# Performance work log

Measured on AMD Instinct MI355X. Metric: run time of the kernel, lower is better.

The kernel has to match this reference:

```python
import jax, jax.numpy as jnp
import numpy as np


def dwconv1d(u, w, b):
    # u: (B, C, L), w: (C, 1, 3) depthwise, padding=1 -> same length
    out = jax.lax.conv_general_dilated(
        u, w, window_strides=(1,), padding=[(1, 1)],
        dimension_numbers=('NCH', 'OIH', 'NCH'),
        feature_group_count=u.shape[1])
    return out + b[None, :, None]


def selective_scan(u, delta, A, Bm, Cm, D, delta_bias):
    # u, delta: (B, KD, L); A: (KD, N); Bm, Cm: (B, K, N, L); D, delta_bias: (KD,)
    Bsz, KD, L = u.shape
    K, N = Bm.shape[1], Bm.shape[2]
    Dg = KD // K
    delta = jax.nn.softplus(delta + delta_bias[None, :, None])
    Bexp = jnp.repeat(Bm, Dg, axis=1)  # (B, KD, N, L)
    Cexp = jnp.repeat(Cm, Dg, axis=1)
    dA = jnp.exp(delta[:, :, None, :] * A[None, :, :, None])        # (B, KD, N, L)
    dBu = delta[:, :, None, :] * Bexp * u[:, :, None, :]            # (B, KD, N, L)

    def step(h, inp):
        a, bu, c = inp
        h = a * h + bu
        return h, jnp.sum(h * c, axis=-1)

    a_t = jnp.moveaxis(dA, -1, 0)
    bu_t = jnp.moveaxis(dBu, -1, 0)
    c_t = jnp.moveaxis(Cexp, -1, 0)
    _, ys = jax.lax.scan(step, jnp.zeros((Bsz, KD, N), u.dtype), (a_t, bu_t, c_t))
    return jnp.moveaxis(ys, 0, -1) + D[None, :, None] * u           # (B, KD, L)


def setup_inputs():
    key = jax.random.key(0)
    ks = jax.random.split(key, 8)
    d_inner, d_state, dt_rank, K = 192, 16, 6, 1
    bincounts = np.array([4096, 3000, 3500, 2500])
    total = int(bincounts.sum())
    max_bin = int(bincounts.max())
    starts = np.concatenate([[0], np.cumsum(bincounts)[:-1]])
    # compute_padding: wrap-around padded gather indices per cloud
    padded_idx = np.concatenate([np.arange(max_bin) % bc + st for bc, st in zip(bincounts, starts)])
    # crop-back indices into the (B*max_bin) padded layout
    valid_idx = np.concatenate([i * max_bin + np.arange(bc) for i, bc in enumerate(bincounts)])
    order = np.stack([np.random.RandomState(0).permutation(total)])
    inverse = np.argsort(order, axis=1)
    x = jax.random.normal(ks[0], (d_inner, total), jnp.float32)
    x_proj_weight = jax.random.normal(ks[1], (K, dt_rank + 2 * d_state, d_inner), jnp.float32) * 0.05
    dt_projs_weight = jax.random.normal(ks[2], (K, d_inner, dt_rank), jnp.float32) * 0.1
    dt_projs_bias = jax.random.normal(ks[3], (K, d_inner), jnp.float32) * 0.1
    A_logs = jnp.log(jnp.tile(jnp.arange(1, d_state + 1, dtype=jnp.float32), (K * d_inner, 1)))
    Ds = jnp.ones((K * d_inner,), jnp.float32)
    conv_w = jax.random.normal(ks[4], (K * d_inner, 1, 3), jnp.float32) * 0.2
    conv_b = jnp.zeros((K * d_inner,), jnp.float32)
    ln_gamma = jnp.ones((d_inner,), jnp.float32)
    ln_beta = jnp.zeros((d_inner,), jnp.float32)
    return {
        'x': x, 'x_proj_weight': x_proj_weight, 'dt_projs_weight': dt_projs_weight,
        'dt_projs_bias': dt_projs_bias, 'A_logs': A_logs, 'Ds': Ds,
        'conv_w': conv_w, 'conv_b': conv_b, 'ln_gamma': ln_gamma, 'ln_beta': ln_beta,
        'order': jnp.asarray(order, jnp.int32), 'inverse': jnp.asarray(inverse, jnp.int32),
        'padded_idx': jnp.asarray(padded_idx, jnp.int32),
        'valid_idx': jnp.asarray(valid_idx, jnp.int32), 'max_bin': max_bin,
    }


def reference(x, x_proj_weight, dt_projs_weight, dt_projs_bias, A_logs, Ds,
              conv_w, conv_b, ln_gamma, ln_beta,
              order, inverse, padded_idx, valid_idx, max_bin):
    K, Dch, R = dt_projs_weight.shape
    N = A_logs.shape[1]
    BM = padded_idx.shape[0]
    Bsz = BM // max_bin
    # multi-directional gather with offset padding: x[:, order[k]][:, padded_idx]
    idx = jnp.take(order, padded_idx, axis=1)                       # (K, B*max_bin)
    xs = jnp.take(x, idx, axis=1)                                   # (Dch, K, B*max_bin)
    xs = xs.transpose(1, 0, 2).reshape(K, Dch, Bsz, max_bin).transpose(2, 0, 1, 3)  # (B,K,D,L)
    x_dbl = jnp.einsum('bkdl,kcd->bkcl', xs, x_proj_weight)         # (B,K,R+2N,L)
    dts, Bs, Cs = jnp.split(x_dbl, [R, R + N], axis=2)
    dts = jnp.einsum('bkrl,kdr->bkdl', dts, dt_projs_weight)
    u = xs.reshape(Bsz, K * Dch, max_bin)
    delta = dts.reshape(Bsz, K * Dch, max_bin)
    A = -jnp.exp(A_logs)
    u = dwconv1d(u, conv_w, conv_b)  # conv1d applied after x_dbl/dts, before scan
    ys = selective_scan(u, delta, A, Bs, Cs, Ds, dt_projs_bias.reshape(-1))  # (B, K*Dch, L)
    # crop padding per cloud and concat along points
    ys = ys.reshape(Bsz, K, Dch, max_bin).transpose(1, 2, 0, 3).reshape(K, Dch, BM)
    ys = jnp.take(ys, valid_idx, axis=2)                            # (K, Dch, total)
    # K == 1, y_proj_weight is None -> scatter back through inverse permutation
    y = jnp.take(ys[0], inverse[0], axis=1)                         # (Dch, total)
    y = y.T                                                         # (total, Dch)
    mu = jnp.mean(y, axis=-1, keepdims=True)
    var = jnp.var(y, axis=-1, keepdims=True)
    y = (y - mu) / jnp.sqrt(var + 1e-5) * ln_gamma + ln_beta        # LayerNorm(d_inner)
    return y
```

## Files before the change

### kernel.cpp

```cpp
#include <hip/hip_runtime.h>
#include <math.h>

#define DINNER 192
#define NST    16
#define RNK    6
#define LSEQ   4096
#define BSZ    4
#define TOTAL  13096
#define BMPAD  16384
#define CL     32
#define MAXC   128
#define NSTATE 3072
#define NCHAIN 12288
#define NB32   410

#define BC_OF(b)  ((b)==0?4096:(b)==1?3000:(b)==2?3500:2500)
#define QST_OF(b) ((b)==0?0:(b)==1?4096:(b)==2?7096:10596)
#define NCB_OF(b) ((b)==0?128:(b)==1?94:(b)==2?110:79)

__device__ float  g_xs[(size_t)TOTAL * DINNER];
__device__ float  g_BC[(size_t)TOTAL * 32];
__device__ float  g_dt[(size_t)TOTAL * 8];
__device__ float2 g_PQ[(size_t)BSZ * MAXC * NSTATE];
__device__ float  g_hin[(size_t)BSZ * MAXC * NSTATE];

#define POWER_TREE(e, a)                                                   \
    { float e1 = (e);                                                      \
      float e2 = e1*e1, e4 = e2*e2, e8 = e4*e4;                            \
      a[0]=e1;      a[1]=e2;      a[2]=e2*e1;   a[3]=e4;                   \
      a[4]=e4*e1;   a[5]=e4*e2;   a[6]=e4*a[2]; a[7]=e8;                   \
      a[8]=e8*e1;   a[9]=e8*e2;   a[10]=e8*a[2];a[11]=e8*e4;               \
      a[12]=e8*a[4];a[13]=e8*a[5];a[14]=e8*a[6];a[15]=e8*e8; }

__global__ __launch_bounds__(256) void kA(
    const float* __restrict__ x, const float* __restrict__ W,
    const int* __restrict__ inverse)
{
    const int P0 = blockIdx.x * 32;
    const int npts = min(32, TOTAL - P0);
    const int t = threadIdx.x;

    __shared__ float sx[32 * 193];
    __shared__ float sW[38 * DINNER];
    __shared__ int   sg[32];

    if (t < 32) sg[t] = (t < npts) ? inverse[P0 + t] : 0;

    float xt[24];
    #pragma unroll
    for (int k = 0; k < 24; ++k) {
        int idx = t + k * 256;
        int j = idx & 31, d = idx >> 5;
        xt[k] = (j < npts) ? x[(size_t)d * TOTAL + P0 + j] : 0.f;
    }
    float wt[29];
    #pragma unroll
    for (int k = 0; k < 29; ++k) {
        int idx = t + k * 256;
        wt[k] = (idx < 38 * DINNER) ? W[idx] : 0.f;
    }
    #pragma unroll
    for (int k = 0; k < 24; ++k) {
        int idx = t + k * 256;
        sx[(idx & 31) * 193 + (idx >> 5)] = xt[k];
    }
    #pragma unroll
    for (int k = 0; k < 29; ++k) {
        int idx = t + k * 256;
        if (idx < 38 * DINNER) sW[idx] = wt[k];
    }
    __syncthreads();

    for (int idx = t; idx < npts * 48; idx += 256) {
        int j = idx / 48, q = idx - j * 48;
        const float* sp = &sx[j * 193 + q * 4];
        float4 v = {sp[0], sp[1], sp[2], sp[3]};
        *(float4*)&g_xs[(size_t)sg[j] * DINNER + q * 4] = v;
    }

    const int j = t & 31, cw = t >> 5;
    float acc[5] = {0.f, 0.f, 0.f, 0.f, 0.f};
    for (int dt0 = 0; dt0 < DINNER; dt0 += 16) {
        float xr[16];
        #pragma unroll
        for (int q = 0; q < 16; ++q) xr[q] = sx[j * 193 + dt0 + q];
        #pragma unroll
        for (int k = 0; k < 5; ++k) {
            const int c = cw + 8 * k;
            if (c < RNK + 2 * NST) {
                const float4* wr = (const float4*)&sW[c * DINNER + dt0];
                float4 w0 = wr[0], w1 = wr[1], w2 = wr[2], w3 = wr[3];
                float a = acc[k];
                a += xr[0]*w0.x + xr[1]*w0.y + xr[2]*w0.z + xr[3]*w0.w;
                a += xr[4]*w1.x + xr[5]*w1.y + xr[6]*w1.z + xr[7]*w1.w;
                a += xr[8]*w2.x + xr[9]*w2.y + xr[10]*w2.z + xr[11]*w2.w;
                a += xr[12]*w3.x + xr[13]*w3.y + xr[14]*w3.z + xr[15]*w3.w;
                acc[k] = a;
            }
        }
    }
    if (j < npts) {
        const int g = sg[j];
        #pragma unroll
        for (int k = 0; k < 5; ++k) {
            const int c = cw + 8 * k;
            if (c < RNK)                g_dt[(size_t)g * 8 + c] = acc[k];
            else if (c < RNK + 2 * NST) g_BC[(size_t)g * 32 + (c - RNK)] = acc[k];
        }
    }
}

__global__ __launch_bounds__(192) void k2_scan1(
    const float* __restrict__ A_logs, const float* __restrict__ conv_w,
    const float* __restrict__ conv_b, const float* __restrict__ dtW,
    const float* __restrict__ dtB)
{
    const int blk = blockIdx.x;
    const int b = blk >> 7;
    const int chunk = blk & (MAXC - 1);
    const int bc = BC_OF(b), qst = QST_OF(b), ncb = NCB_OF(b);
    if (chunk >= ncb) return;
    const int l0 = chunk * CL;
    const int steps = min(CL, bc - l0);
    const int t = threadIdx.x;

    __shared__ float sB[CL * NST];
    __shared__ float sdt[CL * 8];

    float xr[CL + 2];
    #pragma unroll
    for (int k = 0; k < CL + 2; ++k) {
        int pos = l0 - 1 + k;
        bool v = (k < steps + 2) && (pos >= 0) && (pos < LSEQ);
        int pw = (pos >= bc) ? pos - bc : pos;
        xr[k] = v ? g_xs[(size_t)(qst + pw) * DINNER + t] : 0.f;
    }
    float bv[3];
    #pragma unroll
    for (int k = 0; k < 3; ++k) {
        int idx = t + k * 192;
        bv[k] = (idx < steps * NST)
              ? g_BC[(size_t)(qst + l0 + (idx >> 4)) * 32 + (idx & 15)] : 0.f;
    }
    float dv[2];
    #pragma unroll
    for (int k = 0; k < 2; ++k) {
        int idx = t + k * 192;
        dv[k] = (idx < steps * 8) ? g_dt[(size_t)(qst + l0) * 8 + idx] : 0.f;
    }
    #pragma unroll
    for (int k = 0; k < 3; ++k) {
        int idx = t + k * 192;
        if (idx < CL * NST) sB[idx] = bv[k];
    }
    #pragma unroll
    for (int k = 0; k < 2; ++k) {
        int idx = t + k * 192;
        if (idx < CL * 8) sdt[idx] = dv[k];
    }
    __syncthreads();

    float Av[16];
    {
        const float4* A4 = (const float4*)(A_logs + t * NST);
        #pragma unroll
        for (int q = 0; q < 4; ++q) {
            float4 v = A4[q];
            Av[q*4+0] = -__expf(v.x); Av[q*4+1] = -__expf(v.y);
            Av[q*4+2] = -__expf(v.z); Av[q*4+3] = -__expf(v.w);
        }
    }
    const float Av0 = Av[0];
    bool fast = true;
    #pragma unroll
    for (int n = 0; n < 16; ++n)
        fast = fast && (fabsf(Av[n] - (float)(n + 1) * Av0) <= 1e-4f * (float)(n + 1));

    float wdt[RNK];
    #pragma unroll
    for (int r = 0; r < RNK; ++r) wdt[r] = dtW[t * RNK + r];
    const float bdel = dtB[t];
    const float cw0 = conv_w[t*3+0], cw1 = conv_w[t*3+1], cw2 = conv_w[t*3+2];
    const float cb = conv_b[t];

    float h[16];
    #pragma unroll
    for (int n = 0; n < 16; ++n) h[n] = 0.f;
    float delsum = 0.f;

    #pragma unroll
    for (int i = 0; i < CL; ++i) {
        float u = fmaf(cw0, xr[i], fmaf(cw1, xr[i + 1], fmaf(cw2, xr[i + 2], cb)));
        float da = bdel;
        #pragma unroll
        for (int r = 0; r < RNK; ++r) da = fmaf(wdt[r], sdt[i * 8 + r], da);
        float del = (da > 20.f) ? da : log1pf(__expf(da));
        if (i >= steps) del = 0.f;
        float du = del * u;
        delsum += del;
        const float4* b4 = (const float4*)&sB[i * NST];
        float4 B0 = b4[0], B1 = b4[1], B2 = b4[2], B3 = b4[3];
        const float Bv[16] = {B0.x,B0.y,B0.z,B0.w, B1.x,B1.y,B1.z,B1.w,
                              B2.x,B2.y,B2.z,B2.w, B3.x,B3.y,B3.z,B3.w};
        if (fast) {
            float a[16];
            POWER_TREE(__expf(del * Av0), a);
            #pragma unroll
            for (int n = 0; n < 16; ++n) h[n] = fmaf(a[n], h[n], Bv[n] * du);
        } else {
            #pragma unroll
            for (int n = 0; n < 16; ++n) {
                float a = __expf(del * Av[n]);
                h[n] = fmaf(a, h[n], Bv[n] * du);
            }
        }
    }

    float4* o4 = (float4*)(g_PQ + (size_t)(b * MAXC + chunk) * NSTATE + t * 16);
    #pragma unroll
    for (int k = 0; k < 8; ++k) {
        float P0v = __expf(Av[2*k]   * delsum);
        float P1v = __expf(Av[2*k+1] * delsum);
        o4[k] = make_float4(P0v, h[2*k], P1v, h[2*k+1]);
    }
}

__global__ __launch_bounds__(128) void k3_comb()
{
    const int gid = blockIdx.x * 128 + threadIdx.x;
    const int b = gid / NSTATE;
    const int s = gid - b * NSTATE;
    const int ncb = NCB_OF(b);
    float h = 0.f;
    for (int c0 = 0; c0 < MAXC; c0 += 16) {
        if (c0 >= ncb) break;
        float2 v[16];
        #pragma unroll
        for (int k = 0; k < 16; ++k) {
            int c = c0 + k;
            v[k] = (c < ncb) ? g_PQ[(size_t)(b * MAXC + c) * NSTATE + s]
                             : make_float2(1.f, 0.f);
        }
        #pragma unroll
        for (int k = 0; k < 16; ++k) {
            int c = c0 + k;
            if (c < ncb) g_hin[(size_t)(b * MAXC + c) * NSTATE + s] = h;
            h = fmaf(v[k].x, h, v[k].y);
        }
    }
}

__global__ __launch_bounds__(192) void k4_scan2(
    const float* __restrict__ A_logs, const float* __restrict__ conv_w,
    const float* __restrict__ conv_b, const float* __restrict__ dtW,
    const float* __restrict__ dtB, const float* __restrict__ Ds,
    const int* __restrict__ order, const float* __restrict__ gamma,
    const float* __restrict__ beta, float* __restrict__ out)
{
    const int blk = blockIdx.x;
    const int b = blk >> 7;
    const int chunk = blk & (MAXC - 1);
    const int bc = BC_OF(b), qst = QST_OF(b), ncb = NCB_OF(b);
    if (chunk >= ncb) return;
    const int l0 = chunk * CL;
    const int steps = min(CL, bc - l0);
    const int t = threadIdx.x;

    __shared__ float sy[CL * DINNER];
    __shared__ float sBC[CL * 32];
    __shared__ float sdt[CL * 8];

    float xr[CL + 2];
    #pragma unroll
    for (int k = 0; k < CL + 2; ++k) {
        int pos = l0 - 1 + k;
        bool v = (k < steps + 2) && (pos >= 0) && (pos < LSEQ);
        int pw = (pos >= bc) ? pos - bc : pos;
        xr[k] = v ? g_xs[(size_t)(qst + pw) * DINNER + t] : 0.f;
    }
    float bcv[6];
    #pragma unroll
    for (int k = 0; k < 6; ++k) {
        int idx = t + k * 192;
        bcv[k] = (idx < steps * 32) ? g_BC[(size_t)(qst + l0) * 32 + idx] : 0.f;
    }
    float dv[2];
    #pragma unroll
    for (int k = 0; k < 2; ++k) {
        int idx = t + k * 192;
        dv[k] = (idx < steps * 8) ? g_dt[(size_t)(qst + l0) * 8 + idx] : 0.f;
    }
    float h[16];
    {
        const float4* h4 = (const float4*)(g_hin + (size_t)(b * MAXC + chunk) * NSTATE + t * 16);
        #pragma unroll
        for (int q = 0; q < 4; ++q) *(float4*)&h[q * 4] = h4[q];
    }
    #pragma unroll
    for (int k = 0; k < 6; ++k) {
        int idx = t + k * 192;
        if (idx < CL * 32) sBC[idx] = bcv[k];
    }
    #pragma unroll
    for (int k = 0; k < 2; ++k) {
        int idx = t + k * 192;
        if (idx < CL * 8) sdt[idx] = dv[k];
    }
    __syncthreads();

    float Av[16];
    {
        const float4* A4 = (const float4*)(A_logs + t * NST);
        #pragma unroll
        for (int q = 0; q < 4; ++q) {
            float4 v = A4[q];
            Av[q*4+0] = -__expf(v.x); Av[q*4+1] = -__expf(v.y);
            Av[q*4+2] = -__expf(v.z); Av[q*4+3] = -__expf(v.w);
        }
    }
    const float Av0 = Av[0];
    bool fast = true;
    #pragma unroll
    for (int n = 0; n < 16; ++n)
        fast = fast && (fabsf(Av[n] - (float)(n + 1) * Av0) <= 1e-4f * (float)(n + 1));

    float wdt[RNK];
    #pragma unroll
    for (int r = 0; r < RNK; ++r) wdt[r] = dtW[t * RNK + r];
    const float bdel = dtB[t];
    const float cw0 = conv_w[t*3+0], cw1 = conv_w[t*3+1], cw2 = conv_w[t*3+2];
    const float cb = conv_b[t];
    const float Dd = Ds[t];

    #pragma unroll
    for (int i = 0; i < CL; ++i) {
        float u = fmaf(cw0, xr[i], fmaf(cw1, xr[i + 1], fmaf(cw2, xr[i + 2], cb)));
        float da = bdel;
        #pragma unroll
        for (int r = 0; r < RNK; ++r) da = fmaf(wdt[r], sdt[i * 8 + r], da);
        float del = (da > 20.f) ? da : log1pf(__expf(da));
        if (i >= steps) del = 0.f;
        float du = del * u;
        const float4* b4 = (const float4*)&sBC[i * 32];
        float4 B0 = b4[0], B1 = b4[1], B2 = b4[2], B3 = b4[3];
        float4 C0 = b4[4], C1 = b4[5], C2 = b4[6], C3 = b4[7];
        const float Bv[16] = {B0.x,B0.y,B0.z,B0.w, B1.x,B1.y,B1.z,B1.w,
                              B2.x,B2.y,B2.z,B2.w, B3.x,B3.y,B3.z,B3.w};
        const float Cv[16] = {C0.x,C0.y,C0.z,C0.w, C1.x,C1.y,C1.z,C1.w,
                              C2.x,C2.y,C2.z,C2.w, C3.x,C3.y,C3.z,C3.w};
        float y = Dd * u;
        if (fast) {
            float a[16];
            POWER_TREE(__expf(del * Av0), a);
            #pragma unroll
            for (int n = 0; n < 16; ++n) {
                h[n] = fmaf(a[n], h[n], Bv[n] * du);
                y = fmaf(h[n], Cv[n], y);
            }
        } else {
            #pragma unroll
            for (int n = 0; n < 16; ++n) {
                float a = __expf(del * Av[n]);
                h[n] = fmaf(a, h[n], Bv[n] * du);
                y = fmaf(h[n], Cv[n], y);
            }
        }
        sy[i * DINNER + t] = y;
    }
    __syncthreads();

    const int wv = t >> 6;
    const int lane = t & 63;
    for (int i = wv; i < steps; i += 3) {
        const float v0 = sy[i * DINNER + lane];
        const float v1 = sy[i * DINNER + 64 + lane];
        const float v2 = sy[i * DINNER + 128 + lane];
        float s  = v0 + v1 + v2;
        float s2 = v0 * v0 + v1 * v1 + v2 * v2;
        #pragma unroll
        for (int off = 1; off < 64; off <<= 1) {
            s  += __shfl_xor(s,  off);
            s2 += __shfl_xor(s2, off);
        }
        const float mu   = s / (float)DINNER;
        const float var  = s2 / (float)DINNER - mu * mu;
        const float rstd = rsqrtf(var + 1e-5f);
        const int p = order[qst + l0 + i];
        float* orow = out + (size_t)p * DINNER;
        orow[lane]       = (v0 - mu) * rstd * gamma[lane]       + beta[lane];
        orow[lane + 64]  = (v1 - mu) * rstd * gamma[lane + 64]  + beta[lane + 64];
        orow[lane + 128] = (v2 - mu) * rstd * gamma[lane + 128] + beta[lane + 128];
    }
}

extern "C" void kernel_launch(void* const* d_in, const int* in_sizes, int n_in,
                              void* d_out, int out_size, void* d_ws, size_t ws_size,
                              hipStream_t stream) {
    const float* x       = (const float*)d_in[0];
    const float* W       = (const float*)d_in[1];
    const float* dtW     = (const float*)d_in[2];
    const float* dtB     = (const float*)d_in[3];
    const float* A_logs  = (const float*)d_in[4];
    const float* Ds      = (const float*)d_in[5];
    const float* conv_w  = (const float*)d_in[6];
    const float* conv_b  = (const float*)d_in[7];
    const float* gamma   = (const float*)d_in[8];
    const float* beta    = (const float*)d_in[9];
    const int*   order   = (const int*)d_in[10];
    const int*   inverse = (const int*)d_in[11];
    float* outp = (float*)d_out;

    if (in_sizes[0] != TOTAL * DINNER || in_sizes[12] != BMPAD) return;

    kA<<<NB32, 256, 0, stream>>>(x, W, inverse);
    k2_scan1<<<BSZ * MAXC, 192, 0, stream>>>(A_logs, conv_w, conv_b, dtW, dtB);
    k3_comb<<<NCHAIN / 128, 128, 0, stream>>>();
    k4_scan2<<<BSZ * MAXC, 192, 0, stream>>>(A_logs, conv_w, conv_b, dtW, dtB,
                                             Ds, order, gamma, beta, outp);
}
```

Baseline: 175.7 us.

## Fuse chunked scan passes into one kernel with decoupled look-back across chunks

Replaces the three-kernel scan (local chunk scan, chain combine, rescan) with a single kernel. Each block publishes its chunk-local end state and delta sum, signals a flag, then spins on predecessor flags and folds their states into its carry-in before rescanning and applying LayerNorm. This removes two kernel launches and the round trip through global carry buffers. In exchange it depends on inter-block spin-waiting, which is guarded by an occupancy check, adds a serial look-back whose length grows with chunk index, and needs a flag reset placed in kA.

```diff
diff --git a/kernel.cpp b/kernel.cpp
--- a/kernel.cpp
+++ b/kernel.cpp
@@ -18,11 +18,15 @@
 #define QST_OF(b) ((b)==0?0:(b)==1?4096:(b)==2?7096:10596)
 #define NCB_OF(b) ((b)==0?128:(b)==1?94:(b)==2?110:79)
 
+typedef unsigned long long u64;
+
 __device__ float  g_xs[(size_t)TOTAL * DINNER];
 __device__ float  g_BC[(size_t)TOTAL * 32];
 __device__ float  g_dt[(size_t)TOTAL * 8];
 __device__ float2 g_PQ[(size_t)BSZ * MAXC * NSTATE];
 __device__ float  g_hin[(size_t)BSZ * MAXC * NSTATE];
+__device__ u64    g_AG[(size_t)BSZ * MAXC * 9 * 192];
+__device__ int    g_flag[BSZ * MAXC];
 
 #define POWER_TREE(e, a)                                                   \
     { float e1 = (e);                                                      \
@@ -39,6 +43,9 @@
     const int P0 = blockIdx.x * 32;
     const int npts = min(32, TOTAL - P0);
     const int t = threadIdx.x;
+
+    if (blockIdx.x == 0)
+        for (int i = t; i < BSZ * MAXC; i += 256) g_flag[i] = 0;
 
     __shared__ float sx[32 * 193];
     __shared__ float sW[38 * DINNER];
@@ -107,6 +114,233 @@
             if (c < RNK)                g_dt[(size_t)g * 8 + c] = acc[k];
             else if (c < RNK + 2 * NST) g_BC[(size_t)g * 32 + (c - RNK)] = acc[k];
         }
+    }
+}
+
+__global__ __launch_bounds__(192) void k2f(
+    const float* __restrict__ A_logs, const float* __restrict__ conv_w,
+    const float* __restrict__ conv_b, const float* __restrict__ dtW,
+    const float* __restrict__ dtB, const float* __restrict__ Ds,
+    const int* __restrict__ order, const float* __restrict__ gamma,
+    const float* __restrict__ beta, float* __restrict__ out)
+{
+    const int blk = blockIdx.x;
+    const int b = blk >> 7;
+    const int chunk = blk & (MAXC - 1);
+    const int bc = BC_OF(b), qst = QST_OF(b), ncb = NCB_OF(b);
+    if (chunk >= ncb) return;
+    const int l0 = chunk * CL;
+    const int steps = min(CL, bc - l0);
+    const int t = threadIdx.x;
+
+    __shared__ float sy[CL * DINNER];
+    __shared__ float sBC[CL * 32];
+    __shared__ float sdt[CL * 8];
+
+    float xr[CL + 2];
+    #pragma unroll
+    for (int k = 0; k < CL + 2; ++k) {
+        int pos = l0 - 1 + k;
+        bool v = (k < steps + 2) && (pos >= 0) && (pos < LSEQ);
+        int pw = (pos >= bc) ? pos - bc : pos;
+        xr[k] = v ? g_xs[(size_t)(qst + pw) * DINNER + t] : 0.f;
+    }
+    float bcv[6];
+    #pragma unroll
+    for (int k = 0; k < 6; ++k) {
+        int idx = t + k * 192;
+        bcv[k] = (idx < steps * 32) ? g_BC[(size_t)(qst + l0) * 32 + idx] : 0.f;
+    }
+    float dv[2];
+    #pragma unroll
+    for (int k = 0; k < 2; ++k) {
+        int idx = t + k * 192;
+        dv[k] = (idx < steps * 8) ? g_dt[(size_t)(qst + l0) * 8 + idx] : 0.f;
+    }
+    #pragma unroll
+    for (int k = 0; k < 6; ++k) {
+        int idx = t + k * 192;
+        if (idx < CL * 32) sBC[idx] = bcv[k];
+    }
+    #pragma unroll
+    for (int k = 0; k < 2; ++k) {
+        int idx = t + k * 192;
+        if (idx < CL * 8) sdt[idx] = dv[k];
+    }
+    __syncthreads();
+
+    float Av[16];
+    {
+        const float4* A4 = (const float4*)(A_logs + t * NST);
+        #pragma unroll
+        for (int q = 0; q < 4; ++q) {
+            float4 v = A4[q];
+            Av[q*4+0] = -__expf(v.x); Av[q*4+1] = -__expf(v.y);
+            Av[q*4+2] = -__expf(v.z); Av[q*4+3] = -__expf(v.w);
+        }
+    }
+    const float Av0 = Av[0];
+    bool fast = true;
+    #pragma unroll
+    for (int n = 0; n < 16; ++n)
+        fast = fast && (fabsf(Av[n] - (float)(n + 1) * Av0) <= 1e-4f * (float)(n + 1));
+
+    float wdt[RNK];
+    #pragma unroll
+    for (int r = 0; r < RNK; ++r) wdt[r] = dtW[t * RNK + r];
+    const float bdel = dtB[t];
+    const float cw0 = conv_w[t*3+0], cw1 = conv_w[t*3+1], cw2 = conv_w[t*3+2];
+    const float cb = conv_b[t];
+    const float Dd = Ds[t];
+
+    float h[16];
+    #pragma unroll
+    for (int n = 0; n < 16; ++n) h[n] = 0.f;
+    float delsum = 0.f;
+    #pragma unroll
+    for (int i = 0; i < CL; ++i) {
+        float u = fmaf(cw0, xr[i], fmaf(cw1, xr[i + 1], fmaf(cw2, xr[i + 2], cb)));
+        float da = bdel;
+        #pragma unroll
+        for (int r = 0; r < RNK; ++r) da = fmaf(wdt[r], sdt[i * 8 + r], da);
+        float del = (da > 20.f) ? da : log1pf(__expf(da));
+        if (i >= steps) del = 0.f;
+        float du = del * u;
+        delsum += del;
+        const float4* b4 = (const float4*)&sBC[i * 32];
+        float4 B0 = b4[0], B1 = b4[1], B2 = b4[2], B3 = b4[3];
+        const float Bv[16] = {B0.x,B0.y,B0.z,B0.w, B1.x,B1.y,B1.z,B1.w,
+                              B2.x,B2.y,B2.z,B2.w, B3.x,B3.y,B3.z,B3.w};
+        if (fast) {
+            float a[16];
+            POWER_TREE(__expf(del * Av0), a);
+            #pragma unroll
+            for (int n = 0; n < 16; ++n) h[n] = fmaf(a[n], h[n], Bv[n] * du);
+        } else {
+            #pragma unroll
+            for (int n = 0; n < 16; ++n) {
+                float a = __expf(del * Av[n]);
+                h[n] = fmaf(a, h[n], Bv[n] * du);
+            }
+        }
+    }
+
+    {
+        float2* base = (float2*)g_AG + ((size_t)(b * MAXC + chunk) * 9) * 192 + t;
+        #pragma unroll
+        for (int p = 0; p < 8; ++p)
+            base[p * 192] = make_float2(h[2 * p], h[2 * p + 1]);
+        base[8 * 192] = make_float2(delsum, 0.f);
+    }
+    __threadfence();
+    __syncthreads();
+    if (t == 0)
+        __hip_atomic_store(&g_flag[b * MAXC + chunk], 1,
+                           __ATOMIC_RELEASE, __HIP_MEMORY_SCOPE_AGENT);
+
+    float Qs[16], Ps[16];
+    #pragma unroll
+    for (int n = 0; n < 16; ++n) { Qs[n] = 0.f; Ps[n] = 1.f; }
+    int jc = chunk - 1;
+    while (jc >= 0) {
+        const int nb = (jc >= 3) ? 4 : (jc + 1);
+        if (t == 0) {
+            for (int k = 0; k < nb; ++k)
+                while (__hip_atomic_load(&g_flag[b * MAXC + (jc - k)],
+                                         __ATOMIC_ACQUIRE,
+                                         __HIP_MEMORY_SCOPE_AGENT) == 0) {}
+        }
+        __syncthreads();
+        float q[4][16], dsj[4];
+        for (int k = 0; k < nb; ++k) {
+            const u64* src = g_AG + ((size_t)(b * MAXC + (jc - k)) * 9) * 192 + t;
+            #pragma unroll
+            for (int p = 0; p < 8; ++p) {
+                u64 w = __hip_atomic_load(src + p * 192, __ATOMIC_RELAXED,
+                                          __HIP_MEMORY_SCOPE_AGENT);
+                float2 f = *(float2*)&w;
+                q[k][2 * p] = f.x; q[k][2 * p + 1] = f.y;
+            }
+            u64 wd = __hip_atomic_load(src + 8 * 192, __ATOMIC_RELAXED,
+                                       __HIP_MEMORY_SCOPE_AGENT);
+            dsj[k] = ((float2*)&wd)->x;
+        }
+        for (int k = 0; k < nb; ++k) {
+            float Pj[16];
+            if (fast) { POWER_TREE(__expf(dsj[k] * Av0), Pj); }
+            else {
+                #pragma unroll
+                for (int n = 0; n < 16; ++n) Pj[n] = __expf(dsj[k] * Av[n]);
+            }
+            #pragma unroll
+            for (int n = 0; n < 16; ++n) {
+                Qs[n] = fmaf(Ps[n], q[k][n], Qs[n]);
+                Ps[n] *= Pj[n];
+            }
+        }
+        jc -= nb;
+    }
+
+    #pragma unroll
+    for (int n = 0; n < 16; ++n) h[n] = Qs[n];
+    #pragma unroll
+    for (int i = 0; i < CL; ++i) {
+        float u = fmaf(cw0, xr[i], fmaf(cw1, xr[i + 1], fmaf(cw2, xr[i + 2], cb)));
+        float da = bdel;
+        #pragma unroll
+        for (int r = 0; r < RNK; ++r) da = fmaf(wdt[r], sdt[i * 8 + r], da);
+        float del = (da > 20.f) ? da : log1pf(__expf(da));
+        if (i >= steps) del = 0.f;
+        float du = del * u;
+        const float4* b4 = (const float4*)&sBC[i * 32];
+        float4 B0 = b4[0], B1 = b4[1], B2 = b4[2], B3 = b4[3];
+        float4 C0 = b4[4], C1 = b4[5], C2 = b4[6], C3 = b4[7];
+        const float Bv[16] = {B0.x,B0.y,B0.z,B0.w, B1.x,B1.y,B1.z,B1.w,
+                              B2.x,B2.y,B2.z,B2.w, B3.x,B3.y,B3.z,B3.w};
+        const float Cv[16] = {C0.x,C0.y,C0.z,C0.w, C1.x,C1.y,C1.z,C1.w,
+                              C2.x,C2.y,C2.z,C2.w, C3.x,C3.y,C3.z,C3.w};
+        float y = Dd * u;
+        if (fast) {
+            float a[16];
+            POWER_TREE(__expf(del * Av0), a);
+            #pragma unroll
+            for (int n = 0; n < 16; ++n) {
+                h[n] = fmaf(a[n], h[n], Bv[n] * du);
+                y = fmaf(h[n], Cv[n], y);
+            }
+        } else {
+            #pragma unroll
+            for (int n = 0; n < 16; ++n) {
+                float a = __expf(del * Av[n]);
+                h[n] = fmaf(a, h[n], Bv[n] * du);
+                y = fmaf(h[n], Cv[n], y);
+            }
+        }
+        sy[i * DINNER + t] = y;
+    }
+    __syncthreads();
+
+    const int wv = t >> 6;
+    const int lane = t & 63;
+    for (int i = wv; i < steps; i += 3) {
+        const float v0 = sy[i * DINNER + lane];
+        const float v1 = sy[i * DINNER + 64 + lane];
+        const float v2 = sy[i * DINNER + 128 + lane];
+        float s  = v0 + v1 + v2;
+        float s2 = v0 * v0 + v1 * v1 + v2 * v2;
+        #pragma unroll
+        for (int off = 1; off < 64; off <<= 1) {
+            s  += __shfl_xor(s,  off);
+            s2 += __shfl_xor(s2, off);
+        }
+        const float mu   = s / (float)DINNER;
+        const float var  = s2 / (float)DINNER - mu * mu;
+        const float rstd = rsqrtf(var + 1e-5f);
+        const int p = order[qst + l0 + i];
+        float* orow = out + (size_t)p * DINNER;
+        orow[lane]       = (v0 - mu) * rstd * gamma[lane]       + beta[lane];
+        orow[lane + 64]  = (v1 - mu) * rstd * gamma[lane + 64]  + beta[lane + 64];
+        orow[lane + 128] = (v2 - mu) * rstd * gamma[lane + 128] + beta[lane + 128];
     }
 }
 
@@ -413,8 +647,17 @@
     if (in_sizes[0] != TOTAL * DINNER || in_sizes[12] != BMPAD) return;
 
     kA<<<NB32, 256, 0, stream>>>(x, W, inverse);
-    k2_scan1<<<BSZ * MAXC, 192, 0, stream>>>(A_logs, conv_w, conv_b, dtW, dtB);
-    k3_comb<<<NCHAIN / 128, 128, 0, stream>>>();
-    k4_scan2<<<BSZ * MAXC, 192, 0, stream>>>(A_logs, conv_w, conv_b, dtW, dtB,
-                                             Ds, order, gamma, beta, outp);
+
+    int maxb = 0;
+    hipError_t oe = hipOccupancyMaxActiveBlocksPerMultiprocessor(
+        &maxb, (const void*)k2f, 192, 0);
+    if (oe == hipSuccess && maxb >= 2) {
+        k2f<<<BSZ * MAXC, 192, 0, stream>>>(A_logs, conv_w, conv_b, dtW, dtB,
+                                            Ds, order, gamma, beta, outp);
+    } else {
+        k2_scan1<<<BSZ * MAXC, 192, 0, stream>>>(A_logs, conv_w, conv_b, dtW, dtB);
+        k3_comb<<<NCHAIN / 128, 128, 0, stream>>>();
+        k4_scan2<<<BSZ * MAXC, 192, 0, stream>>>(A_logs, conv_w, conv_b, dtW, dtB,
+                                                 Ds, order, gamma, beta, outp);
+    }
 }
```

New measurement: 176.5 us. No clear change (+0.5%).
